# Optimization experiments

Measured on AMD Instinct MI355X. Metric: run time of the kernel, lower is better.

## Reference

```python
import jax, jax.numpy as jnp
import numpy as np

S, I = 64, 128

def _images():
    # 27 periodic image offsets in [-1,0,1]^3, same ordering as the torch module
    r = jnp.arange(-1.0, 2.0)
    a, b, c = jnp.meshgrid(r, r, r, indexing='ij')
    return jnp.stack([a.ravel(), b.ravel(), c.ravel()], axis=-1)  # [27,3]


def setup_inputs() -> dict:
    key = jax.random.key(0)
    k1, k2, k3 = jax.random.split(key, 3)
    fcoords1 = jax.random.uniform(k1, (S, I, 3), dtype=jnp.float32)
    fcoords2 = jax.random.uniform(k2, (S, I, 3), dtype=jnp.float32)
    matrix = jax.random.normal(k3, (S, 3, 3), dtype=jnp.float32)
    return {"fcoords1": fcoords1, "fcoords2": fcoords2, "matrix": matrix}


def reference(fcoords1, fcoords2, matrix):
    eps = jnp.asarray(1e-10, fcoords1.dtype)
    imgs = _images().astype(matrix.dtype)                      # [27,3]
    cart_coords = jnp.einsum('sij,sjk->sik', fcoords1 % 1, matrix)  # [S,I,3]
    cart1 = cart_coords
    cart2 = jnp.einsum('sij,sjk->sik', fcoords2 % 1, matrix)        # [S,I,3]
    cart_im = jnp.einsum('ij,sjk->sik', imgs, matrix)               # [S,27,3]
    # diff[s,i,j,m,:] = cart2[s,i] - cart1[s,j] + cart_im[s,m]
    d = (cart2[:, :, None, None, :] - cart1[:, None, :, None, :]
         + cart_im[:, None, None, :, :])                            # [S,I,I,27,3]
    dm = jnp.min(jnp.sum(d * d, axis=-1), axis=-1)                  # [S,I,I]
    return jnp.sqrt(dm + eps), cart_coords
```

## Files before the change

### kernel.cpp

```cpp
#include <hip/hip_runtime.h>
#include <math.h>

constexpr int S_ = 64;
constexpr int I_ = 128;
constexpr int PAIRS = I_ * I_;
constexpr int TILES = 8;
constexpr int PAIRS_PER_TILE = PAIRS / TILES;
constexpr int THREADS = 256;
constexpr int PPT = PAIRS_PER_TILE / THREADS;

__device__ __forceinline__ float rfl(float x) {
    return __int_as_float(__builtin_amdgcn_readfirstlane(__float_as_int(x)));
}

__global__ __launch_bounds__(THREADS) void diffdist_kernel(
    const float* __restrict__ f1,
    const float* __restrict__ f2,
    const float* __restrict__ M,
    float* __restrict__ out)
{
    const int s    = blockIdx.x >> 3;
    const int tile = blockIdx.x & (TILES - 1);
    const int tid  = threadIdx.x;

    __shared__ float c1[I_][3];
    __shared__ float c2[I_][3];

    const float* Ms = M + s * 9;
    const float m00 = Ms[0], m01 = Ms[1], m02 = Ms[2];
    const float m10 = Ms[3], m11 = Ms[4], m12 = Ms[5];
    const float m20 = Ms[6], m21 = Ms[7], m22 = Ms[8];

    {
        const int row = tid & (I_ - 1);
        const float* fsrc = (tid < I_) ? f1 : f2;
        const float* p = fsrc + (size_t)(s * I_ + row) * 3;
        float a = p[0]; a -= floorf(a);
        float b = p[1]; b -= floorf(b);
        float g = p[2]; g -= floorf(g);
        float x = fmaf(a, m00, fmaf(b, m10, g * m20));
        float y = fmaf(a, m01, fmaf(b, m11, g * m21));
        float z = fmaf(a, m02, fmaf(b, m12, g * m22));
        if (tid < I_) {
            c1[row][0] = x; c1[row][1] = y; c1[row][2] = z;
            if (tile == 0) {
                float* o2 = out + (size_t)S_ * PAIRS + (size_t)(s * I_ + row) * 3;
                o2[0] = x; o2[1] = y; o2[2] = z;
            }
        } else {
            c2[row][0] = x; c2[row][1] = y; c2[row][2] = z;
        }
    }

    constexpr int IA[13] = {0, 0, 0, 0,  1,  1, 1,  1, 1, 1,  1, 1, 1};
    constexpr int IB[13] = {0, 1, 1, 1, -1, -1,-1,  0, 0, 0,  1, 1, 1};
    constexpr int IC[13] = {1,-1, 0, 1, -1,  0, 1, -1, 0, 1, -1, 0, 1};

    float t2x[13], t2y[13], t2z[13], cc[13];
    #pragma unroll
    for (int m = 0; m < 13; ++m) {
        const float fa = (float)IA[m], fb = (float)IB[m], fc = (float)IC[m];
        const float tx = fa * m00 + fb * m10 + fc * m20;
        const float ty = fa * m01 + fb * m11 + fc * m21;
        const float tz = fa * m02 + fb * m12 + fc * m22;
        cc[m]  = rfl(fmaf(tx, tx, fmaf(ty, ty, tz * tz)));
        t2x[m] = rfl(tx + tx);
        t2y[m] = rfl(ty + ty);
        t2z[m] = rfl(tz + tz);
    }

    __syncthreads();

    const int j  = tid & (I_ - 1);
    const int hi = tid >> 7;
    const float c1x = c1[j][0], c1y = c1[j][1], c1z = c1[j][2];

    float* od = out + (size_t)s * PAIRS + tile * PAIRS_PER_TILE;

    #pragma unroll
    for (int p = 0; p < PPT; ++p) {
        const int ii = tile * 16 + p * 2 + hi;
        const float bx = c2[ii][0] - c1x;
        const float by = c2[ii][1] - c1y;
        const float bz = c2[ii][2] - c1z;
        const float n  = fmaf(bx, bx, fmaf(by, by, bz * bz));

        float best = 0.0f;
        #pragma unroll
        for (int m = 0; m < 13; ++m) {
            const float u  = fmaf(bx, t2x[m], fmaf(by, t2y[m], bz * t2z[m]));
            const float d1 = cc[m] + u;
            const float d2 = cc[m] - u;
            best = fminf(best, fminf(d1, d2));
        }
        od[p * THREADS + tid] = sqrtf(fmaxf(n + best, 0.0f) + 1e-10f);
    }
}

extern "C" void kernel_launch(void* const* d_in, const int* in_sizes, int n_in,
                              void* d_out, int out_size, void* d_ws, size_t ws_size,
                              hipStream_t stream) {
    const float* f1 = (const float*)d_in[0];
    const float* f2 = (const float*)d_in[1];
    const float* M  = (const float*)d_in[2];
    float* out = (float*)d_out;

    dim3 grid(S_ * TILES);
    dim3 block(THREADS);
    diffdist_kernel<<<grid, block, 0, stream>>>(f1, f2, M, out);
}
```

Baseline: 10.69 us.

## Precompute per-row and per-column image terms, reduce inner loop to packed adds

```diff
diff --git a/kernel.cpp b/kernel.cpp
--- a/kernel.cpp
+++ b/kernel.cpp
@@ -5,13 +5,13 @@
 constexpr int I_ = 128;
 constexpr int PAIRS = I_ * I_;
 constexpr int TILES = 8;
-constexpr int PAIRS_PER_TILE = PAIRS / TILES;
+constexpr int PPTILE = PAIRS / TILES;
 constexpr int THREADS = 256;
-constexpr int PPT = PAIRS_PER_TILE / THREADS;
+constexpr int PPT = PPTILE / THREADS;
+constexpr int IPT = 2 * PPT;
+constexpr int NM = 14;
 
-__device__ __forceinline__ float rfl(float x) {
-    return __int_as_float(__builtin_amdgcn_readfirstlane(__float_as_int(x)));
-}
+typedef float v2f __attribute__((ext_vector_type(2)));
 
 __global__ __launch_bounds__(THREADS) void diffdist_kernel(
     const float* __restrict__ f1,
@@ -23,77 +23,87 @@
     const int tile = blockIdx.x & (TILES - 1);
     const int tid  = threadIdx.x;
 
-    __shared__ float c1[I_][3];
-    __shared__ float c2[I_][3];
+    __shared__ float4 c1v[I_];
+    __shared__ float4 c2v[I_];
+    __shared__ float4 tc[NM];
+    __shared__ v2f    PP[IPT][NM];
 
     const float* Ms = M + s * 9;
     const float m00 = Ms[0], m01 = Ms[1], m02 = Ms[2];
     const float m10 = Ms[3], m11 = Ms[4], m12 = Ms[5];
     const float m20 = Ms[6], m21 = Ms[7], m22 = Ms[8];
 
+    if (tid < NM) {
+        const int m = tid;
+        const float fa = (float)(m >= 5);
+        const float fb = (float)(((m + 1) / 3 + 1) % 3 - 1);
+        const float fc = (float)((m + 1) % 3 - 1);
+        const float tx = fa * m00 + fb * m10 + fc * m20;
+        const float ty = fa * m01 + fb * m11 + fc * m21;
+        const float tz = fa * m02 + fb * m12 + fc * m22;
+        tc[m] = make_float4(tx + tx, ty + ty, tz + tz,
+                            fmaf(tx, tx, fmaf(ty, ty, tz * tz)));
+    }
+
     {
         const int row = tid & (I_ - 1);
-        const float* fsrc = (tid < I_) ? f1 : f2;
-        const float* p = fsrc + (size_t)(s * I_ + row) * 3;
+        const float* p = ((tid < I_) ? f1 : f2) + (size_t)(s * I_ + row) * 3;
         float a = p[0]; a -= floorf(a);
         float b = p[1]; b -= floorf(b);
         float g = p[2]; g -= floorf(g);
-        float x = fmaf(a, m00, fmaf(b, m10, g * m20));
-        float y = fmaf(a, m01, fmaf(b, m11, g * m21));
-        float z = fmaf(a, m02, fmaf(b, m12, g * m22));
+        const float x = fmaf(a, m00, fmaf(b, m10, g * m20));
+        const float y = fmaf(a, m01, fmaf(b, m11, g * m21));
+        const float z = fmaf(a, m02, fmaf(b, m12, g * m22));
+        const float w = fmaf(x, x, fmaf(y, y, z * z));
         if (tid < I_) {
-            c1[row][0] = x; c1[row][1] = y; c1[row][2] = z;
+            c1v[row] = make_float4(x, y, z, w);
             if (tile == 0) {
                 float* o2 = out + (size_t)S_ * PAIRS + (size_t)(s * I_ + row) * 3;
                 o2[0] = x; o2[1] = y; o2[2] = z;
             }
         } else {
-            c2[row][0] = x; c2[row][1] = y; c2[row][2] = z;
+            c2v[row] = make_float4(x, y, z, w);
         }
     }
-
-    constexpr int IA[13] = {0, 0, 0, 0,  1,  1, 1,  1, 1, 1,  1, 1, 1};
-    constexpr int IB[13] = {0, 1, 1, 1, -1, -1,-1,  0, 0, 0,  1, 1, 1};
-    constexpr int IC[13] = {1,-1, 0, 1, -1,  0, 1, -1, 0, 1, -1, 0, 1};
-
-    float t2x[13], t2y[13], t2z[13], cc[13];
-    #pragma unroll
-    for (int m = 0; m < 13; ++m) {
-        const float fa = (float)IA[m], fb = (float)IB[m], fc = (float)IC[m];
-        const float tx = fa * m00 + fb * m10 + fc * m20;
-        const float ty = fa * m01 + fb * m11 + fc * m21;
-        const float tz = fa * m02 + fb * m12 + fc * m22;
-        cc[m]  = rfl(fmaf(tx, tx, fmaf(ty, ty, tz * tz)));
-        t2x[m] = rfl(tx + tx);
-        t2y[m] = rfl(ty + ty);
-        t2z[m] = rfl(tz + tz);
-    }
-
     __syncthreads();
 
     const int j  = tid & (I_ - 1);
     const int hi = tid >> 7;
-    const float c1x = c1[j][0], c1y = c1[j][1], c1z = c1[j][2];
+    const float4 cj = c1v[j];
+    const float hx = cj.x + cj.x, hy = cj.y + cj.y, hz = cj.z + cj.z;
+    v2f Q[NM];
+    #pragma unroll
+    for (int m = 0; m < NM; ++m) {
+        const float4 t = tc[m];
+        const float wj = fmaf(cj.x, t.x, fmaf(cj.y, t.y, cj.z * t.z));
+        Q[m] = (v2f){cj.w - wj, cj.w + wj};
+    }
 
-    float* od = out + (size_t)s * PAIRS + tile * PAIRS_PER_TILE;
+    if (tid < IPT * NM) {
+        const int il = tid / NM;
+        const int m  = tid - il * NM;
+        const float4 ci = c2v[tile * IPT + il];
+        const float4 t  = tc[m];
+        const float vi   = fmaf(ci.x, t.x, fmaf(ci.y, t.y, ci.z * t.z));
+        const float base = ci.w + t.w;
+        PP[il][m] = (v2f){base + vi, base - vi};
+    }
+    __syncthreads();
 
+    float* od = out + (size_t)s * PAIRS + tile * PPTILE;
     #pragma unroll
     for (int p = 0; p < PPT; ++p) {
-        const int ii = tile * 16 + p * 2 + hi;
-        const float bx = c2[ii][0] - c1x;
-        const float by = c2[ii][1] - c1y;
-        const float bz = c2[ii][2] - c1z;
-        const float n  = fmaf(bx, bx, fmaf(by, by, bz * bz));
-
-        float best = 0.0f;
+        const int il = p * 2 + hi;
+        const float4 ci = c2v[tile * IPT + il];
+        const float G = fmaf(ci.x, hx, fmaf(ci.y, hy, ci.z * hz));
+        v2f e = PP[il][0] + Q[0];
+        float best = fminf(e.x, e.y);
         #pragma unroll
-        for (int m = 0; m < 13; ++m) {
-            const float u  = fmaf(bx, t2x[m], fmaf(by, t2y[m], bz * t2z[m]));
-            const float d1 = cc[m] + u;
-            const float d2 = cc[m] - u;
-            best = fminf(best, fminf(d1, d2));
+        for (int m = 1; m < NM; ++m) {
+            const v2f d = PP[il][m] + Q[m];
+            best = fminf(best, fminf(d.x, d.y));
         }
-        od[p * THREADS + tid] = sqrtf(fmaxf(n + best, 0.0f) + 1e-10f);
+        od[p * THREADS + tid] = sqrtf(fmaxf(best - G, 0.0f) + 1e-10f);
     }
 }
 
```

New measurement: 10.70 us. About the same (+0.1%).
